# Kernel optimization log

Hardware: AMD Instinct MI355X
Metric: run time of the kernel (lower is better)

## Reference

```python
import jax, jax.numpy as jnp
import numpy as np

N_NODES = 400_000
N_EDGES = 1_600_000
N_GRAPHS = 16_384
MOL_DIM = 32
META_DIM = 16
HIDDEN = 64
NUM_SPECIES = 50
FUSION = 2 * HIDDEN + HIDDEN + 16  # mean+max pool (128) + meta (64) + species emb (16) = 208


def setup_inputs() -> dict:
    key = jax.random.key(0)
    ks = jax.random.split(key, 20)
    s = lambda *sh: sh
    inp = {
        "x": jax.random.normal(ks[0], (N_NODES, MOL_DIM), jnp.float32),
        "metadata": jax.random.normal(ks[1], (N_GRAPHS, META_DIM), jnp.float32),
        "edge_index": jax.random.randint(ks[2], (2, N_EDGES), 0, N_NODES),
        "batch": jnp.sort(jax.random.randint(ks[3], (N_NODES,), 0, N_GRAPHS)),
        "species_id": jax.random.randint(ks[4], (N_GRAPHS,), 0, NUM_SPECIES),
        # GCN layer params
        "W1": jax.random.normal(ks[5], (MOL_DIM, HIDDEN), jnp.float32) / np.sqrt(MOL_DIM),
        "b1": jnp.zeros((HIDDEN,), jnp.float32),
        "W2": jax.random.normal(ks[6], (HIDDEN, HIDDEN), jnp.float32) / np.sqrt(HIDDEN),
        "b2": jnp.zeros((HIDDEN,), jnp.float32),
        "W3": jax.random.normal(ks[7], (HIDDEN, HIDDEN), jnp.float32) / np.sqrt(HIDDEN),
        "b3": jnp.zeros((HIDDEN,), jnp.float32),
        # meta encoder
        "Wm": jax.random.normal(ks[8], (META_DIM, HIDDEN), jnp.float32) / np.sqrt(META_DIM),
        "bm": jnp.zeros((HIDDEN,), jnp.float32),
        "species_emb": jax.random.normal(ks[9], (NUM_SPECIES, 16), jnp.float32),
        # predictor
        "Wp1": jax.random.normal(ks[10], (FUSION, 64), jnp.float32) / np.sqrt(FUSION),
        "bp1": jnp.zeros((64,), jnp.float32),
        "Wp2": jax.random.normal(ks[11], (64, 1), jnp.float32) / 8.0,
        "bp2": jnp.zeros((1,), jnp.float32),
    }
    return inp


def _gcn_conv(x, W, b, row, col, dinv):
    # x' = D^{-1/2}(A+I)D^{-1/2} x W + b  (PyG GCNConv with self-loops)
    h = x @ W                                   # [N, out]
    norm = dinv[row] * dinv[col]                # [E]
    msg = norm[:, None] * h[col]                # [E, out]
    agg = jax.ops.segment_sum(msg, row, num_segments=x.shape[0])
    agg = agg + (dinv * dinv)[:, None] * h      # self-loop term
    return agg + b


def reference(x, metadata, edge_index, batch, species_id,
              W1, b1, W2, b2, W3, b3, Wm, bm, species_emb, Wp1, bp1, Wp2, bp2):
    row, col = edge_index[0], edge_index[1]
    deg = jax.ops.segment_sum(jnp.ones_like(row, jnp.float32), row,
                              num_segments=N_NODES) + 1.0  # +1 self loop
    dinv = jax.lax.rsqrt(deg)

    h = jax.nn.relu(_gcn_conv(x, W1, b1, row, col, dinv))
    h = jax.nn.relu(_gcn_conv(h, W2, b2, row, col, dinv))
    h = jax.nn.relu(_gcn_conv(h, W3, b3, row, col, dinv))

    counts = jax.ops.segment_sum(jnp.ones((N_NODES,), jnp.float32), batch,
                                 num_segments=N_GRAPHS)
    mean = jax.ops.segment_sum(h, batch, num_segments=N_GRAPHS) / \
           jnp.maximum(counts, 1.0)[:, None]
    mx = jax.ops.segment_max(h, batch, num_segments=N_GRAPHS)
    mx = jnp.where(counts[:, None] > 0, mx, 0.0)
    graph_embed = jnp.concatenate([mean, mx], axis=1)     # [G, 128]

    meta = jax.nn.relu(metadata @ Wm + bm)                 # [G, 64]
    meta_embed = jnp.concatenate([meta, species_emb[species_id]], axis=1)

    fused = jnp.concatenate([graph_embed, meta_embed], axis=1)  # [G, 208]
    out = jax.nn.relu(fused @ Wp1 + bp1) @ Wp2 + bp2       # dropout off (eval)
    return out
```

## Files before the change

kernel.cpp:

```cpp
#include <hip/hip_runtime.h>
#include <hip/hip_bf16.h>

#define N_NODES 400000
#define N_EDGES 1600000
#define N_GRAPHS 16384
#define CHUNK 32
#define NCHUNK (N_NODES / CHUNK)

#define BSHIFT 11
#define BKT_N (1 << BSHIFT)
#define NBKT ((N_NODES + BKT_N - 1) >> BSHIFT)
#define BIN_CHUNK 4096

typedef __attribute__((ext_vector_type(8))) short bf16x8;
typedef __attribute__((ext_vector_type(4))) float f32x4;
typedef unsigned short bfu;

__device__ __forceinline__ float rlane(float x, int k) {
    return __int_as_float(__builtin_amdgcn_readlane(__float_as_int(x), k));
}
__device__ __forceinline__ int rlanei(int x, int k) {
    return __builtin_amdgcn_readlane(x, k);
}

__device__ __forceinline__ short f2bf(float x) {
    unsigned u = __float_as_uint(x);
    unsigned r = (u + 0x7fffu + ((u >> 16) & 1u)) >> 16;
    return (short)r;
}
__device__ __forceinline__ float bf2f(short b) {
    return __uint_as_float(((unsigned)(unsigned short)b) << 16);
}
__device__ __forceinline__ float bfu2f(bfu b) {
    return __uint_as_float(((unsigned)b) << 16);
}

__global__ __launch_bounds__(256) void k_bcnt(const int* __restrict__ rows,
                                              int* __restrict__ bkt, int E) {
    __shared__ int l[NBKT];
    const int t = threadIdx.x;
    for (int i = t; i < NBKT; i += 256) l[i] = 0;
    __syncthreads();
    const int e0 = blockIdx.x * BIN_CHUNK;
#pragma unroll
    for (int k = 0; k < 16; ++k) {
        int e = e0 + k * 256 + t;
        if (e < E) atomicAdd(&l[rows[e] >> BSHIFT], 1);
    }
    __syncthreads();
    for (int i = t; i < NBKT; i += 256)
        if (l[i]) atomicAdd(&bkt[i], l[i]);
}

__global__ void k_bscan(const int* __restrict__ bkt, int* __restrict__ bbase,
                        int* __restrict__ bcur) {
    __shared__ int s[256];
    const int t = threadIdx.x;
    int v = (t < NBKT) ? bkt[t] : 0;
    s[t] = v; __syncthreads();
    for (int off = 1; off < 256; off <<= 1) {
        int x = (t >= off) ? s[t - off] : 0;
        __syncthreads();
        s[t] += x;
        __syncthreads();
    }
    int excl = s[t] - v;
    if (t < NBKT) { bbase[t] = excl; bcur[t] = excl; }
    if (t == NBKT) bbase[NBKT] = excl;
}

__global__ __launch_bounds__(256) void k_bin(const int* __restrict__ rows,
                                             const int* __restrict__ cols,
                                             int* __restrict__ bcur,
                                             int2* __restrict__ tmp, int E) {
    __shared__ int lcnt[NBKT];
    __shared__ int lbase[NBKT];
    const int t = threadIdx.x;
    const int e0 = blockIdx.x * BIN_CHUNK;
    for (int i = t; i < NBKT; i += 256) lcnt[i] = 0;
    __syncthreads();
    int r[16];
#pragma unroll
    for (int k = 0; k < 16; ++k) {
        int e = e0 + k * 256 + t;
        r[k] = (e < E) ? rows[e] : -1;
        if (r[k] >= 0) atomicAdd(&lcnt[r[k] >> BSHIFT], 1);
    }
    __syncthreads();
    for (int i = t; i < NBKT; i += 256) lbase[i] = atomicAdd(&bcur[i], lcnt[i]);
    __syncthreads();
    for (int i = t; i < NBKT; i += 256) lcnt[i] = 0;
    __syncthreads();
#pragma unroll
    for (int k = 0; k < 16; ++k) {
        int e = e0 + k * 256 + t;
        if (r[k] >= 0) {
            int b = r[k] >> BSHIFT;
            int p = lbase[b] + atomicAdd(&lcnt[b], 1);
            tmp[p] = make_int2(r[k], cols[e]);
        }
    }
}

__global__ __launch_bounds__(256) void k_csr(const int2* __restrict__ tmp,
                                             const int* __restrict__ bbase,
                                             int* __restrict__ row_ptr,
                                             float* __restrict__ dinv,
                                             int* __restrict__ colsOut,
                                             int N, int E) {
    __shared__ int lcnt[BKT_N];
    __shared__ int lofs[BKT_N];
    __shared__ int tsum[256];
    const int t = threadIdx.x;
    const int b = blockIdx.x;
    const int r0 = b << BSHIFT;
    const int S = bbase[b];
    const int T = bbase[b + 1];
    for (int i = t; i < BKT_N; i += 256) lcnt[i] = 0;
    __syncthreads();
    for (int e = S + t; e < T; e += 256) atomicAdd(&lcnt[tmp[e].x - r0], 1);
    __syncthreads();
    const int base8 = t * 8;
    int vals[8];
    int run = 0;
#pragma unroll
    for (int k = 0; k < 8; ++k) { vals[k] = run; run += lcnt[base8 + k]; }
    tsum[t] = run;
    __syncthreads();
    for (int off = 1; off < 256; off <<= 1) {
        int x = (t >= off) ? tsum[t - off] : 0;
        __syncthreads();
        tsum[t] += x;
        __syncthreads();
    }
    const int texcl = tsum[t] - run;
#pragma unroll
    for (int k = 0; k < 8; ++k) lofs[base8 + k] = texcl + vals[k];
    __syncthreads();
    for (int i = t; i < BKT_N; i += 256) {
        int node = r0 + i;
        if (node < N) {
            row_ptr[node] = S + lofs[i];
            dinv[node] = rsqrtf((float)lcnt[i] + 1.0f);
        }
    }
    if (b == 0 && t == 0) row_ptr[N] = E;
    __syncthreads();
    for (int e = S + t; e < T; e += 256) {
        int2 rc = tmp[e];
        int pos = S + atomicAdd(&lofs[rc.x - r0], 1);
        colsOut[pos] = rc.y;
    }
}

__global__ void k_gb(const int* __restrict__ batch, int* __restrict__ gstart,
                     int N, int G) {
    int i = blockIdx.x * blockDim.x + threadIdx.x;
    if (i <= N) {
        int b = (i < N) ? batch[i] : G;
        int prev = (i == 0) ? -1 : batch[i - 1];
        for (int g = prev + 1; g <= b; ++g) gstart[g] = i;
    }
}

template <int IN_D, bool PRESCALE, bool ABF16>
__global__ __launch_bounds__(256, 4) void k_gemm_mfma(
        const void* __restrict__ in_, const float* __restrict__ W,
        const float* __restrict__ dinv, bfu* __restrict__ out, int nTiles) {
    constexpr int KT = IN_D / 32;
    const int lane = threadIdx.x & 63;
    const int m = lane & 15;
    const int q = lane >> 4;

    bf16x8 Bhi[4][KT], Blo[4][KT];
#pragma unroll
    for (int nt = 0; nt < 4; ++nt) {
#pragma unroll
        for (int kt = 0; kt < KT; ++kt) {
#pragma unroll
            for (int j = 0; j < 8; ++j) {
                int k = kt * 32 + q * 8 + j;
                float w = W[k * 64 + nt * 16 + m];
                short hi = f2bf(w);
                Bhi[nt][kt][j] = hi;
                Blo[nt][kt][j] = f2bf(w - bf2f(hi));
            }
        }
    }

    const int wv = (blockIdx.x * 256 + threadIdx.x) >> 6;
    const int nwv = (gridDim.x * 256) >> 6;

    for (int tile = wv; tile < nTiles; tile += nwv) {
        const int node0 = tile * 16;
        f32x4 C[4];
#pragma unroll
        for (int nt = 0; nt < 4; ++nt) C[nt] = (f32x4){0.f, 0.f, 0.f, 0.f};

        if (ABF16) {
            const bfu* rowb = (const bfu*)in_ + (size_t)(node0 + m) * IN_D + q * 8;
            bf16x8 A[KT];
#pragma unroll
            for (int kt = 0; kt < KT; ++kt) A[kt] = *(const bf16x8*)(rowb + kt * 32);
#pragma unroll
            for (int nt = 0; nt < 4; ++nt) {
#pragma unroll
                for (int kt = 0; kt < KT; ++kt) {
                    C[nt] = __builtin_amdgcn_mfma_f32_16x16x32_bf16(A[kt], Bhi[nt][kt], C[nt], 0, 0, 0);
                    C[nt] = __builtin_amdgcn_mfma_f32_16x16x32_bf16(A[kt], Blo[nt][kt], C[nt], 0, 0, 0);
                }
            }
        } else {
            const float dv = PRESCALE ? dinv[node0 + m] : 1.0f;
            const float* rowp = (const float*)in_ + (size_t)(node0 + m) * IN_D + q * 8;
            bf16x8 Ahi[KT], Alo[KT];
#pragma unroll
            for (int kt = 0; kt < KT; ++kt) {
                f32x4 a0 = *(const f32x4*)(rowp + kt * 32);
                f32x4 a1 = *(const f32x4*)(rowp + kt * 32 + 4);
#pragma unroll
                for (int j = 0; j < 4; ++j) {
                    float xx = PRESCALE ? dv * a0[j] : a0[j];
                    short hi = f2bf(xx);
                    Ahi[kt][j] = hi;
                    Alo[kt][j] = f2bf(xx - bf2f(hi));
                }
#pragma unroll
                for (int j = 0; j < 4; ++j) {
                    float xx = PRESCALE ? dv * a1[j] : a1[j];
                    short hi = f2bf(xx);
                    Ahi[kt][4 + j] = hi;
                    Alo[kt][4 + j] = f2bf(xx - bf2f(hi));
                }
            }
#pragma unroll
            for (int nt = 0; nt < 4; ++nt) {
#pragma unroll
                for (int kt = 0; kt < KT; ++kt) {
                    C[nt] = __builtin_amdgcn_mfma_f32_16x16x32_bf16(Ahi[kt], Bhi[nt][kt], C[nt], 0, 0, 0);
                    C[nt] = __builtin_amdgcn_mfma_f32_16x16x32_bf16(Ahi[kt], Blo[nt][kt], C[nt], 0, 0, 0);
                    C[nt] = __builtin_amdgcn_mfma_f32_16x16x32_bf16(Alo[kt], Bhi[nt][kt], C[nt], 0, 0, 0);
                }
            }
        }

        bfu* op = out + (size_t)node0 * 64;
#pragma unroll
        for (int nt = 0; nt < 4; ++nt) {
#pragma unroll
            for (int r = 0; r < 4; ++r) {
                op[(size_t)(q * 4 + r) * 64 + nt * 16 + m] = (bfu)f2bf(C[nt][r]);
            }
        }
    }
}

template <int POOL>
__global__ __launch_bounds__(256, 8) void k_agg_seg(
        const bfu* __restrict__ M, const float* __restrict__ bias,
        const int* __restrict__ row_ptr, const int* __restrict__ cols,
        const float* __restrict__ dinv, const int* __restrict__ batch,
        bfu* __restrict__ out, float* __restrict__ psum,
        float* __restrict__ pmax) {
    const int lane = threadIdx.x & 63;
    int wid = (blockIdx.x * blockDim.x + threadIdx.x) >> 6;
    wid = __builtin_amdgcn_readfirstlane(wid);
    const int nw = (gridDim.x * blockDim.x) >> 6;
    const float b = bias[lane];
    const bfu* Ml = M + lane;

    for (int c = wid; c < NCHUNK; c += nw) {
        const int i0 = c * CHUNK;
        const int rpn = row_ptr[i0 + min(lane, CHUNK - 1) + 1];
        const int S = row_ptr[i0];
        const int ne = rlanei(rpn, CHUNK - 1) - S;
        const float dvv = dinv[i0 + min(lane, CHUNK - 1)];
        const int bvv = POOL ? batch[i0 + min(lane, CHUNK - 1)] : 0;

        int node = 0;
        int bnd = rlanei(rpn, 0) - S;
        float acc = 0.0f;
        float selfA = bfu2f(Ml[(size_t)i0 * 64]);
        float selfB = bfu2f(Ml[(size_t)(i0 + 1) * 64]);
        float selfC = bfu2f(Ml[(size_t)(i0 + 2) * 64]);
        int gcur = POOL ? rlanei(bvv, 0) : 0;
        float rsum = 0.0f, rmax = 0.0f;

        auto flush = [&]() {
            if (POOL) {
                atomicAdd(&psum[(size_t)gcur * 64 + lane], rsum);
                atomicMax((int*)&pmax[(size_t)gcur * 64 + lane], __float_as_int(rmax));
            }
        };
        auto finalize = [&]() {
            const float d = rlane(dvv, node);
            const float h = fmaxf(fmaf(d, selfA + acc, b), 0.0f);
            if (POOL) {
                const int g = rlanei(bvv, node);
                if (g != gcur) { flush(); gcur = g; rsum = 0.0f; rmax = 0.0f; }
                rsum += h;
                rmax = fmaxf(rmax, h);
            } else {
                out[(size_t)(i0 + node) * 64 + lane] = (bfu)f2bf(d * h);
            }
            acc = 0.0f;
            selfA = selfB;
            selfB = selfC;
            if (node + 3 < CHUNK) selfC = bfu2f(Ml[(size_t)(i0 + node + 3) * 64]);
            ++node;
            if (node < CHUNK) bnd = rlanei(rpn, node) - S;
        };

        if (ne > 0) {
            int bidx = 0;
            int a0 = S + lane, a1 = S + 64 + lane;
            int colv0 = (a0 < S + ne) ? cols[a0] : 0;
            int colv1 = (a1 < S + ne) ? cols[a1] : 0;
            unsigned ubuf[16];
#pragma unroll
            for (int k = 0; k < 16; ++k) {
                int e = min(k, ne - 1);
                int cc = rlanei(colv0, e);
                ubuf[k] = Ml[(size_t)cc * 64];
            }

            int j = 0;
            while (j + 16 <= ne) {
#pragma unroll
                for (int k = 0; k < 16; ++k) {
                    const int jj = j + k;
                    if ((jj & 63) == 0 && jj != 0) {
                        colv0 = colv1;
                        ++bidx;
                        int ad = S + (bidx + 1) * 64 + lane;
                        colv1 = (ad < S + ne) ? cols[ad] : 0;
                    }
                    while (jj == bnd) finalize();
                    acc += __uint_as_float(ubuf[k] << 16);
                    int ec = min(jj + 16, ne - 1);
                    int src = ((ec >> 6) == bidx) ? colv0 : colv1;
                    int cc = rlanei(src, ec & 63);
                    ubuf[k] = Ml[(size_t)cc * 64];
                }
                j += 16;
            }
            for (; j < ne; ++j) {
                while (j == bnd) finalize();
                acc += __uint_as_float(ubuf[j & 15] << 16);
            }
        }
        while (node < CHUNK) finalize();
        flush();
    }
}

__global__ __launch_bounds__(256) void k_asm(
        const float* __restrict__ psum, const float* __restrict__ pmax,
        const int* __restrict__ gstart, const float* __restrict__ metadata,
        const int* __restrict__ species, const float* __restrict__ emb,
        const float* __restrict__ Wm, const float* __restrict__ bm,
        float* __restrict__ fused, int G) {
    const int lane = threadIdx.x & 63;
    int wv = (blockIdx.x * blockDim.x + threadIdx.x) >> 6;
    const int nw = (gridDim.x * blockDim.x) >> 6;
    const float bmr = bm[lane];
    float wmr[16];
#pragma unroll
    for (int k = 0; k < 16; ++k) wmr[k] = Wm[k * 64 + lane];
    for (int g = wv; g < G; g += nw) {
        float gc = (float)(gstart[g + 1] - gstart[g]);
        float mean = psum[(size_t)g * 64 + lane] / fmaxf(gc, 1.0f);
        float mx = pmax[(size_t)g * 64 + lane];
        float md = lane < 16 ? metadata[(size_t)g * 16 + lane] : 0.0f;
        float mval = bmr;
#pragma unroll
        for (int k = 0; k < 16; ++k) mval = fmaf(rlane(md, k), wmr[k], mval);
        mval = fmaxf(mval, 0.0f);
        const int sid = species[g];
        float* fr = fused + (size_t)g * 224;
        fr[lane] = mean;
        fr[64 + lane] = mx;
        fr[128 + lane] = mval;
        if (lane < 16) fr[192 + lane] = emb[(size_t)sid * 16 + lane];
        else if (lane < 32) fr[192 + lane] = 0.0f;
    }
}

__global__ __launch_bounds__(256, 2) void k_pred_mfma(
        const float* __restrict__ fused, const float* __restrict__ Wp1,
        const float* __restrict__ bp1, const float* __restrict__ Wp2,
        const float* __restrict__ bp2, float* __restrict__ out, int G) {
    __shared__ __align__(16) short Whi[64 * 232];
    __shared__ __align__(16) short Wlo[64 * 232];
    const int t = threadIdx.x;
    for (int idx = t; idx < 64 * 232; idx += 256) {
        int n = idx / 232;
        int k = idx % 232;
        float w = (k < 208) ? Wp1[(size_t)k * 64 + n] : 0.0f;
        short hi = f2bf(w);
        Whi[n * 232 + k] = hi;
        Wlo[n * 232 + k] = f2bf(w - bf2f(hi));
    }
    __syncthreads();

    const int lane = t & 63;
    const int wave = t >> 6;
    const int m = lane & 15;
    const int q = lane >> 4;
    const int g0 = (blockIdx.x * 4 + wave) * 16;
    if (g0 >= G) return;

    const float* rowp = fused + (size_t)(g0 + m) * 224 + q * 8;

    f32x4 C[4];
#pragma unroll
    for (int nt = 0; nt < 4; ++nt) C[nt] = (f32x4){0.f, 0.f, 0.f, 0.f};

#pragma unroll
    for (int kt = 0; kt < 7; ++kt) {
        f32x4 a0 = *(const f32x4*)(rowp + kt * 32);
        f32x4 a1 = *(const f32x4*)(rowp + kt * 32 + 4);
        bf16x8 Ahi, Alo;
#pragma unroll
        for (int j = 0; j < 4; ++j) {
            short hi = f2bf(a0[j]);
            Ahi[j] = hi;
            Alo[j] = f2bf(a0[j] - bf2f(hi));
        }
#pragma unroll
        for (int j = 0; j < 4; ++j) {
            short hi = f2bf(a1[j]);
            Ahi[4 + j] = hi;
            Alo[4 + j] = f2bf(a1[j] - bf2f(hi));
        }
#pragma unroll
        for (int nt = 0; nt < 4; ++nt) {
            const int boff = (nt * 16 + m) * 232 + kt * 32 + q * 8;
            bf16x8 Bh = *(const bf16x8*)&Whi[boff];
            bf16x8 Bl = *(const bf16x8*)&Wlo[boff];
            C[nt] = __builtin_amdgcn_mfma_f32_16x16x32_bf16(Ahi, Bh, C[nt], 0, 0, 0);
            C[nt] = __builtin_amdgcn_mfma_f32_16x16x32_bf16(Ahi, Bl, C[nt], 0, 0, 0);
            C[nt] = __builtin_amdgcn_mfma_f32_16x16x32_bf16(Alo, Bh, C[nt], 0, 0, 0);
        }
    }

    float wp2r[4], bp1r[4];
#pragma unroll
    for (int nt = 0; nt < 4; ++nt) {
        wp2r[nt] = Wp2[nt * 16 + m];
        bp1r[nt] = bp1[nt * 16 + m];
    }
    const float bp2v = bp2[0];
    float s[4];
#pragma unroll
    for (int r = 0; r < 4; ++r) {
        float acc = 0.0f;
#pragma unroll
        for (int nt = 0; nt < 4; ++nt)
            acc += fmaxf(C[nt][r] + bp1r[nt], 0.0f) * wp2r[nt];
        s[r] = acc;
    }
#pragma unroll
    for (int off = 1; off < 16; off <<= 1) {
#pragma unroll
        for (int r = 0; r < 4; ++r) s[r] += __shfl_xor(s[r], off);
    }
    if (m == 0) {
#pragma unroll
        for (int r = 0; r < 4; ++r) out[g0 + q * 4 + r] = s[r] + bp2v;
    }
}

extern "C" void kernel_launch(void* const* d_in, const int* in_sizes, int n_in,
                              void* d_out, int out_size, void* d_ws, size_t ws_size,
                              hipStream_t stream) {
    const int N = N_NODES, E = N_EDGES, G = N_GRAPHS;

    const float* x        = (const float*)d_in[0];
    const float* metadata = (const float*)d_in[1];
    const int*   ei       = (const int*)d_in[2];
    const int*   batch    = (const int*)d_in[3];
    const int*   species  = (const int*)d_in[4];
    const float* W1 = (const float*)d_in[5];
    const float* b1 = (const float*)d_in[6];
    const float* W2 = (const float*)d_in[7];
    const float* b2 = (const float*)d_in[8];
    const float* W3 = (const float*)d_in[9];
    const float* b3 = (const float*)d_in[10];
    const float* Wm = (const float*)d_in[11];
    const float* bm = (const float*)d_in[12];
    const float* emb = (const float*)d_in[13];
    const float* Wp1 = (const float*)d_in[14];
    const float* bp1 = (const float*)d_in[15];
    const float* Wp2 = (const float*)d_in[16];
    const float* bp2 = (const float*)d_in[17];
    float* out = (float*)d_out;

    char* ws = (char*)d_ws;
    size_t off = 0;
    auto alloc = [&](size_t bytes) -> void* {
        void* p = ws + off;
        off = (off + bytes + 255) & ~(size_t)255;
        return p;
    };
    int*   row_ptr = (int*)alloc((size_t)(N + 1) * 4);
    float* dinv    = (float*)alloc((size_t)N * 4);
    int*   gstart  = (int*)alloc((size_t)(G + 1) * 4);
    int*   bkt     = (int*)alloc((size_t)NBKT * 4);
    int*   bbase   = (int*)alloc((size_t)(NBKT + 1) * 4);
    int*   bcur    = (int*)alloc((size_t)NBKT * 4);
    int*   colsS   = (int*)alloc((size_t)E * 4);
    float* psum    = (float*)alloc((size_t)G * 64 * 4);
    float* pmax    = (float*)alloc((size_t)G * 64 * 4);
    bfu*   Mb      = (bfu*)alloc((size_t)N * 64 * 2);
    bfu*   hb      = (bfu*)alloc((size_t)N * 64 * 2);
    float* fused   = (float*)alloc((size_t)G * 224 * 4);

    int2* tmp = (int2*)Mb;

    const int nbBin = (E + BIN_CHUNK - 1) / BIN_CHUNK;

    hipMemsetAsync(bkt, 0, (size_t)NBKT * 4, stream);
    hipMemsetAsync(psum, 0, (size_t)G * 64 * 4, stream);
    hipMemsetAsync(pmax, 0, (size_t)G * 64 * 4, stream);

    k_bcnt<<<nbBin, 256, 0, stream>>>(ei, bkt, E);
    k_bscan<<<1, 256, 0, stream>>>(bkt, bbase, bcur);
    k_bin<<<nbBin, 256, 0, stream>>>(ei, ei + E, bcur, tmp, E);
    k_csr<<<NBKT, 256, 0, stream>>>(tmp, bbase, row_ptr, dinv, colsS, N, E);
    k_gb<<<(N + 256) / 256 + 1, 256, 0, stream>>>(batch, gstart, N, G);

    const int nTiles = N / 16;
    k_gemm_mfma<32, true, false><<<1563, 256, 0, stream>>>(x, W1, dinv, Mb, nTiles);
    k_agg_seg<0><<<3125, 256, 0, stream>>>(Mb, b1, row_ptr, colsS, dinv, batch,
                                           hb, psum, pmax);
    k_gemm_mfma<64, false, true><<<1563, 256, 0, stream>>>(hb, W2, dinv, Mb, nTiles);
    k_agg_seg<0><<<3125, 256, 0, stream>>>(Mb, b2, row_ptr, colsS, dinv, batch,
                                           hb, psum, pmax);
    k_gemm_mfma<64, false, true><<<1563, 256, 0, stream>>>(hb, W3, dinv, Mb, nTiles);
    k_agg_seg<1><<<3125, 256, 0, stream>>>(Mb, b3, row_ptr, colsS, dinv, batch,
                                           hb, psum, pmax);

    k_asm<<<512, 256, 0, stream>>>(psum, pmax, gstart, metadata, species, emb, Wm, bm,
                                   fused, G);
    k_pred_mfma<<<(G / 16 + 3) / 4, 256, 0, stream>>>(fused, Wp1, bp1, Wp2, bp2, out, G);
}
```

Baseline: 488.3 us.

## Split wavefront into half-waves gathering two edges per step in aggregation

Rewrites the CSR aggregation kernel so each lane handles two bf16 features loaded as a packed 32-bit word, and the two half-waves gather different edges (even and odd) at the same time. Each gather instruction therefore covers two edge rows, halving the number of gather steps per edge list, and the half-wave partial sums are combined with a cross-half shuffle at each node finalize. This adds shuffles, more complex boundary handling when a node ends on an odd edge, and halves the lanes doing atomics and stores. Dynamic indexing of ubuf in the tail loop may spill to scratch.

Measured after the change: 541.0 us. +10.8%, slower.

```diff
diff --git a/kernel.cpp b/kernel.cpp
--- a/kernel.cpp
+++ b/kernel.cpp
@@ -263,11 +263,15 @@
         bfu* __restrict__ out, float* __restrict__ psum,
         float* __restrict__ pmax) {
     const int lane = threadIdx.x & 63;
+    const int c2 = lane & 31;
+    const bool hiHalf = lane >= 32;
     int wid = (blockIdx.x * blockDim.x + threadIdx.x) >> 6;
     wid = __builtin_amdgcn_readfirstlane(wid);
     const int nw = (gridDim.x * blockDim.x) >> 6;
-    const float b = bias[lane];
-    const bfu* Ml = M + lane;
+    const float bx = bias[2 * c2];
+    const float by = bias[2 * c2 + 1];
+    const unsigned* Mw = (const unsigned*)M;
+    unsigned* outU = (unsigned*)out;
 
     for (int c = wid; c < NCHUNK; c += nw) {
         const int i0 = c * CHUNK;
@@ -279,34 +283,45 @@
 
         int node = 0;
         int bnd = rlanei(rpn, 0) - S;
-        float acc = 0.0f;
-        float selfA = bfu2f(Ml[(size_t)i0 * 64]);
-        float selfB = bfu2f(Ml[(size_t)(i0 + 1) * 64]);
-        float selfC = bfu2f(Ml[(size_t)(i0 + 2) * 64]);
+        float accx = 0.f, accy = 0.f;
+        unsigned selfA = Mw[(size_t)i0 * 32 + c2];
+        unsigned selfB = Mw[(size_t)(i0 + 1) * 32 + c2];
+        unsigned selfC = Mw[(size_t)(i0 + 2) * 32 + c2];
         int gcur = POOL ? rlanei(bvv, 0) : 0;
-        float rsum = 0.0f, rmax = 0.0f;
+        float rsx = 0.f, rsy = 0.f, rmx = 0.f, rmy = 0.f;
 
         auto flush = [&]() {
-            if (POOL) {
-                atomicAdd(&psum[(size_t)gcur * 64 + lane], rsum);
-                atomicMax((int*)&pmax[(size_t)gcur * 64 + lane], __float_as_int(rmax));
+            if (POOL && lane < 32) {
+                float* pp = &psum[(size_t)gcur * 64 + 2 * c2];
+                atomicAdd(pp, rsx);
+                atomicAdd(pp + 1, rsy);
+                int* pm = (int*)&pmax[(size_t)gcur * 64 + 2 * c2];
+                atomicMax(pm, __float_as_int(rmx));
+                atomicMax(pm + 1, __float_as_int(rmy));
             }
         };
         auto finalize = [&]() {
             const float d = rlane(dvv, node);
-            const float h = fmaxf(fmaf(d, selfA + acc, b), 0.0f);
+            const float sx = accx + __shfl_xor(accx, 32);
+            const float sy = accy + __shfl_xor(accy, 32);
+            const float slo = __uint_as_float(selfA << 16);
+            const float shi = __uint_as_float(selfA & 0xFFFF0000u);
+            const float hx = fmaxf(fmaf(d, slo + sx, bx), 0.0f);
+            const float hy = fmaxf(fmaf(d, shi + sy, by), 0.0f);
             if (POOL) {
                 const int g = rlanei(bvv, node);
-                if (g != gcur) { flush(); gcur = g; rsum = 0.0f; rmax = 0.0f; }
-                rsum += h;
-                rmax = fmaxf(rmax, h);
+                if (g != gcur) { flush(); gcur = g; rsx = rsy = rmx = rmy = 0.f; }
+                rsx += hx; rsy += hy;
+                rmx = fmaxf(rmx, hx); rmy = fmaxf(rmy, hy);
             } else {
-                out[(size_t)(i0 + node) * 64 + lane] = (bfu)f2bf(d * h);
-            }
-            acc = 0.0f;
+                unsigned pk = (unsigned)(unsigned short)f2bf(d * hx)
+                            | ((unsigned)(unsigned short)f2bf(d * hy) << 16);
+                if (lane < 32) outU[(size_t)(i0 + node) * 32 + c2] = pk;
+            }
+            accx = 0.f; accy = 0.f;
             selfA = selfB;
             selfB = selfC;
-            if (node + 3 < CHUNK) selfC = bfu2f(Ml[(size_t)(i0 + node + 3) * 64]);
+            if (node + 3 < CHUNK) selfC = Mw[(size_t)(i0 + node + 3) * 32 + c2];
             ++node;
             if (node < CHUNK) bnd = rlanei(rpn, node) - S;
         };
@@ -319,34 +334,62 @@
             unsigned ubuf[16];
 #pragma unroll
             for (int k = 0; k < 16; ++k) {
-                int e = min(k, ne - 1);
-                int cc = rlanei(colv0, e);
-                ubuf[k] = Ml[(size_t)cc * 64];
+                int eE = min(2 * k, ne - 1);
+                int eO = min(2 * k + 1, ne - 1);
+                int ccE = rlanei(colv0, eE);
+                int ccO = rlanei(colv0, eO);
+                int cc = hiHalf ? ccO : ccE;
+                ubuf[k] = Mw[(size_t)cc * 32 + c2];
             }
 
             int j = 0;
-            while (j + 16 <= ne) {
+            while (j + 32 <= ne) {
+                if (j && !(j & 63)) {
+                    colv0 = colv1;
+                    ++bidx;
+                    int ad = S + (bidx + 1) * 64 + lane;
+                    colv1 = (ad < S + ne) ? cols[ad] : 0;
+                }
 #pragma unroll
                 for (int k = 0; k < 16; ++k) {
-                    const int jj = j + k;
-                    if ((jj & 63) == 0 && jj != 0) {
-                        colv0 = colv1;
-                        ++bidx;
-                        int ad = S + (bidx + 1) * 64 + lane;
-                        colv1 = (ad < S + ne) ? cols[ad] : 0;
+                    const int jj = j + 2 * k;
+                    const unsigned u = ubuf[k];
+                    int eE = min(jj + 32, ne - 1);
+                    int eO = min(jj + 33, ne - 1);
+                    int ccE = ((eE >> 6) == bidx) ? rlanei(colv0, eE & 63)
+                                                  : rlanei(colv1, eE & 63);
+                    int ccO = ((eO >> 6) == bidx) ? rlanei(colv0, eO & 63)
+                                                  : rlanei(colv1, eO & 63);
+                    int cc = hiHalf ? ccO : ccE;
+                    ubuf[k] = Mw[(size_t)cc * 32 + c2];
+                    const float vlo = __uint_as_float(u << 16);
+                    const float vhi = __uint_as_float(u & 0xFFFF0000u);
+                    while (jj == bnd) finalize();
+                    if (bnd == jj + 1) {
+                        if (!hiHalf) { accx += vlo; accy += vhi; }
+                        do { finalize(); } while (bnd == jj + 1);
+                        if (hiHalf) { accx += vlo; accy += vhi; }
+                    } else {
+                        accx += vlo; accy += vhi;
                     }
-                    while (jj == bnd) finalize();
-                    acc += __uint_as_float(ubuf[k] << 16);
-                    int ec = min(jj + 16, ne - 1);
-                    int src = ((ec >> 6) == bidx) ? colv0 : colv1;
-                    int cc = rlanei(src, ec & 63);
-                    ubuf[k] = Ml[(size_t)cc * 64];
-                }
-                j += 16;
-            }
-            for (; j < ne; ++j) {
-                while (j == bnd) finalize();
-                acc += __uint_as_float(ubuf[j & 15] << 16);
+                }
+                j += 32;
+            }
+            for (int e = j; e < ne; e += 2) {
+                const int k = (e - j) >> 1;
+                const unsigned u = ubuf[k];
+                const float vlo = __uint_as_float(u << 16);
+                const float vhi = __uint_as_float(u & 0xFFFF0000u);
+                while (e == bnd) finalize();
+                if (e + 1 >= ne) {
+                    if (!hiHalf) { accx += vlo; accy += vhi; }
+                } else if (bnd == e + 1) {
+                    if (!hiHalf) { accx += vlo; accy += vhi; }
+                    do { finalize(); } while (bnd == e + 1);
+                    if (hiHalf) { accx += vlo; accy += vhi; }
+                } else {
+                    accx += vlo; accy += vhi;
+                }
             }
         }
         while (node < CHUNK) finalize();
```

## Use atomic work-stealing for aggregation chunks and load column indices uniformly

Applied to the files above, without the earlier changes.

The aggregation kernel now has each wavefront fetch its next 32-node chunk from a global atomic counter (one counter per layer) instead of taking chunks in a fixed grid-stride order, and the grid shrinks to 2048 blocks. This is meant to balance load, since edge counts per chunk vary. Column indices are now read per edge with wave-uniform (scalar) loads instead of being staged in two 64-lane registers and broadcast with readlane, which drops the buffer-rotation logic. The column array is padded with 64 zeroed entries so prefetches past the end stay in bounds. The cost is one atomic per chunk plus more scalar memory traffic for the index reads.

Measured after the change: 1.091 ms. 124% more time.

```diff
diff --git a/kernel.cpp b/kernel.cpp
--- a/kernel.cpp
+++ b/kernel.cpp
@@ -261,18 +261,20 @@
         const int* __restrict__ row_ptr, const int* __restrict__ cols,
         const float* __restrict__ dinv, const int* __restrict__ batch,
         bfu* __restrict__ out, float* __restrict__ psum,
-        float* __restrict__ pmax) {
+        float* __restrict__ pmax, int* __restrict__ ctr) {
     const int lane = threadIdx.x & 63;
-    int wid = (blockIdx.x * blockDim.x + threadIdx.x) >> 6;
-    wid = __builtin_amdgcn_readfirstlane(wid);
-    const int nw = (gridDim.x * blockDim.x) >> 6;
     const float b = bias[lane];
     const bfu* Ml = M + lane;
 
-    for (int c = wid; c < NCHUNK; c += nw) {
+    for (;;) {
+        int cw = 0;
+        if (lane == 0) cw = atomicAdd(ctr, 1);
+        const int c = __builtin_amdgcn_readfirstlane(cw);
+        if (c >= NCHUNK) break;
+
         const int i0 = c * CHUNK;
         const int rpn = row_ptr[i0 + min(lane, CHUNK - 1) + 1];
-        const int S = row_ptr[i0];
+        const int S = __builtin_amdgcn_readfirstlane(row_ptr[i0]);
         const int ne = rlanei(rpn, CHUNK - 1) - S;
         const float dvv = dinv[i0 + min(lane, CHUNK - 1)];
         const int bvv = POOL ? batch[i0 + min(lane, CHUNK - 1)] : 0;
@@ -312,15 +314,10 @@
         };
 
         if (ne > 0) {
-            int bidx = 0;
-            int a0 = S + lane, a1 = S + 64 + lane;
-            int colv0 = (a0 < S + ne) ? cols[a0] : 0;
-            int colv1 = (a1 < S + ne) ? cols[a1] : 0;
             unsigned ubuf[16];
 #pragma unroll
             for (int k = 0; k < 16; ++k) {
-                int e = min(k, ne - 1);
-                int cc = rlanei(colv0, e);
+                const int cc = cols[S + k];
                 ubuf[k] = Ml[(size_t)cc * 64];
             }
 
@@ -329,17 +326,9 @@
 #pragma unroll
                 for (int k = 0; k < 16; ++k) {
                     const int jj = j + k;
-                    if ((jj & 63) == 0 && jj != 0) {
-                        colv0 = colv1;
-                        ++bidx;
-                        int ad = S + (bidx + 1) * 64 + lane;
-                        colv1 = (ad < S + ne) ? cols[ad] : 0;
-                    }
                     while (jj == bnd) finalize();
                     acc += __uint_as_float(ubuf[k] << 16);
-                    int ec = min(jj + 16, ne - 1);
-                    int src = ((ec >> 6) == bidx) ? colv0 : colv1;
-                    int cc = rlanei(src, ec & 63);
+                    const int cc = cols[S + jj + 16];
                     ubuf[k] = Ml[(size_t)cc * 64];
                 }
                 j += 16;
@@ -509,7 +498,8 @@
     int*   bkt     = (int*)alloc((size_t)NBKT * 4);
     int*   bbase   = (int*)alloc((size_t)(NBKT + 1) * 4);
     int*   bcur    = (int*)alloc((size_t)NBKT * 4);
-    int*   colsS   = (int*)alloc((size_t)E * 4);
+    int*   ctr     = (int*)alloc(3 * 4);
+    int*   colsS   = (int*)alloc((size_t)(E + 64) * 4);
     float* psum    = (float*)alloc((size_t)G * 64 * 4);
     float* pmax    = (float*)alloc((size_t)G * 64 * 4);
     bfu*   Mb      = (bfu*)alloc((size_t)N * 64 * 2);
@@ -521,6 +511,8 @@
     const int nbBin = (E + BIN_CHUNK - 1) / BIN_CHUNK;
 
     hipMemsetAsync(bkt, 0, (size_t)NBKT * 4, stream);
+    hipMemsetAsync(ctr, 0, 3 * 4, stream);
+    hipMemsetAsync(colsS + E, 0, 64 * 4, stream);
     hipMemsetAsync(psum, 0, (size_t)G * 64 * 4, stream);
     hipMemsetAsync(pmax, 0, (size_t)G * 64 * 4, stream);
 
@@ -532,14 +524,14 @@
 
     const int nTiles = N / 16;
     k_gemm_mfma<32, true, false><<<1563, 256, 0, stream>>>(x, W1, dinv, Mb, nTiles);
-    k_agg_seg<0><<<3125, 256, 0, stream>>>(Mb, b1, row_ptr, colsS, dinv, batch,
-                                           hb, psum, pmax);
+    k_agg_seg<0><<<2048, 256, 0, stream>>>(Mb, b1, row_ptr, colsS, dinv, batch,
+                                           hb, psum, pmax, ctr);
     k_gemm_mfma<64, false, true><<<1563, 256, 0, stream>>>(hb, W2, dinv, Mb, nTiles);
-    k_agg_seg<0><<<3125, 256, 0, stream>>>(Mb, b2, row_ptr, colsS, dinv, batch,
-                                           hb, psum, pmax);
+    k_agg_seg<0><<<2048, 256, 0, stream>>>(Mb, b2, row_ptr, colsS, dinv, batch,
+                                           hb, psum, pmax, ctr + 1);
     k_gemm_mfma<64, false, true><<<1563, 256, 0, stream>>>(hb, W3, dinv, Mb, nTiles);
-    k_agg_seg<1><<<3125, 256, 0, stream>>>(Mb, b3, row_ptr, colsS, dinv, batch,
-                                           hb, psum, pmax);
+    k_agg_seg<1><<<2048, 256, 0, stream>>>(Mb, b3, row_ptr, colsS, dinv, batch,
+                                           hb, psum, pmax, ctr + 2);
 
     k_asm<<<512, 256, 0, stream>>>(psum, pmax, gstart, metadata, species, emb, Wm, bm,
                                    fused, G);
```

## Interleave two node chunks per wave in GCN aggregation for more loads in flight

Applied to the files above, without the earlier changes.

The aggregation kernel now has each wave process two 32-node chunks at once. It alternates 16-edge gather blocks between two independent ring buffers, so twice as many gathers are outstanding per wave. Launch bounds drop from 8 to 4 waves per SIMD and the grid is halved to match. The grid-stride loop is removed and each wave handles exactly one chunk pair. The aim is more memory-level parallelism to hide gather latency, at the cost of more registers per wave, lower occupancy, and possible imbalance when the two chunks have different edge counts.

Result: slower. 631.8 us (+29.4%).

```diff
diff --git a/kernel.cpp b/kernel.cpp
--- a/kernel.cpp
+++ b/kernel.cpp
@@ -255,103 +255,123 @@
     }
 }
 
+
+#define AGG_FLUSH(sfx)                                                          \
+    if (POOL) {                                                                 \
+        atomicAdd(&psum[(size_t)gcur##sfx * 64 + lane], rsum##sfx);             \
+        atomicMax((int*)&pmax[(size_t)gcur##sfx * 64 + lane],                   \
+                  __float_as_int(rmax##sfx));                                   \
+    }
+
+#define AGG_FINALIZE(sfx) {                                                     \
+    const float d_ = rlane(dvv##sfx, node##sfx);                                \
+    const float h_ = fmaxf(fmaf(d_, selfA##sfx + acc##sfx, b), 0.0f);           \
+    if (POOL) {                                                                 \
+        const int g_ = rlanei(bvv##sfx, node##sfx);                             \
+        if (g_ != gcur##sfx) {                                                  \
+            AGG_FLUSH(sfx);                                                     \
+            gcur##sfx = g_; rsum##sfx = 0.0f; rmax##sfx = 0.0f;                 \
+        }                                                                       \
+        rsum##sfx += h_;                                                        \
+        rmax##sfx = fmaxf(rmax##sfx, h_);                                       \
+    } else {                                                                    \
+        out[(size_t)(i0##sfx + node##sfx) * 64 + lane] = (bfu)f2bf(d_ * h_);    \
+    }                                                                           \
+    acc##sfx = 0.0f;                                                            \
+    selfA##sfx = selfB##sfx;                                                    \
+    selfB##sfx = selfC##sfx;                                                    \
+    if (node##sfx + 3 < CHUNK)                                                  \
+        selfC##sfx = bfu2f(Ml[(size_t)(i0##sfx + node##sfx + 3) * 64]);         \
+    ++node##sfx;                                                                \
+    if (node##sfx < CHUNK) bnd##sfx = rlanei(rpn##sfx, node##sfx) - S##sfx; }
+
+#define AGG_INIT(sfx, cval)                                                     \
+    const int i0##sfx = (cval) * CHUNK;                                         \
+    const int rpn##sfx = row_ptr[i0##sfx + min(lane, CHUNK - 1) + 1];           \
+    const int S##sfx = row_ptr[i0##sfx];                                        \
+    const int ne##sfx = rlanei(rpn##sfx, CHUNK - 1) - S##sfx;                   \
+    const float dvv##sfx = dinv[i0##sfx + min(lane, CHUNK - 1)];                \
+    const int bvv##sfx = POOL ? batch[i0##sfx + min(lane, CHUNK - 1)] : 0;      \
+    int node##sfx = 0;                                                          \
+    int bnd##sfx = rlanei(rpn##sfx, 0) - S##sfx;                                \
+    float acc##sfx = 0.0f;                                                      \
+    float selfA##sfx = bfu2f(Ml[(size_t)i0##sfx * 64]);                         \
+    float selfB##sfx = bfu2f(Ml[(size_t)(i0##sfx + 1) * 64]);                   \
+    float selfC##sfx = bfu2f(Ml[(size_t)(i0##sfx + 2) * 64]);                   \
+    int gcur##sfx = POOL ? rlanei(bvv##sfx, 0) : 0;                             \
+    float rsum##sfx = 0.0f, rmax##sfx = 0.0f;                                   \
+    int bidx##sfx = 0;                                                          \
+    int colv0##sfx = 0, colv1##sfx = 0;                                         \
+    unsigned ubuf##sfx[16];                                                     \
+    int j##sfx = 0;
+
+#define AGG_RING_INIT(sfx)                                                      \
+    if (ne##sfx > 0) {                                                          \
+        int a0_ = S##sfx + lane, a1_ = S##sfx + 64 + lane;                      \
+        colv0##sfx = (a0_ < S##sfx + ne##sfx) ? cols[a0_] : 0;                  \
+        colv1##sfx = (a1_ < S##sfx + ne##sfx) ? cols[a1_] : 0;                  \
+        _Pragma("unroll")                                                       \
+        for (int k_ = 0; k_ < 16; ++k_) {                                       \
+            int e_ = min(k_, ne##sfx - 1);                                      \
+            int cc_ = rlanei(colv0##sfx, e_);                                   \
+            ubuf##sfx[k_] = Ml[(size_t)cc_ * 64];                               \
+        }                                                                       \
+    }
+
+#define AGG_BLOCK16(sfx) {                                                      \
+    _Pragma("unroll")                                                           \
+    for (int k_ = 0; k_ < 16; ++k_) {                                           \
+        const int jj_ = j##sfx + k_;                                            \
+        if ((jj_ & 63) == 0 && jj_ != 0) {                                      \
+            colv0##sfx = colv1##sfx;                                            \
+            ++bidx##sfx;                                                        \
+            int ad_ = S##sfx + (bidx##sfx + 1) * 64 + lane;                     \
+            colv1##sfx = (ad_ < S##sfx + ne##sfx) ? cols[ad_] : 0;              \
+        }                                                                       \
+        while (jj_ == bnd##sfx) AGG_FINALIZE(sfx);                              \
+        acc##sfx += __uint_as_float(ubuf##sfx[k_] << 16);                       \
+        int ec_ = min(jj_ + 16, ne##sfx - 1);                                   \
+        int src_ = ((ec_ >> 6) == bidx##sfx) ? colv0##sfx : colv1##sfx;         \
+        int cc_ = rlanei(src_, ec_ & 63);                                       \
+        ubuf##sfx[k_] = Ml[(size_t)cc_ * 64];                                   \
+    }                                                                           \
+    j##sfx += 16; }
+
+#define AGG_TAIL(sfx) {                                                         \
+    for (; j##sfx < ne##sfx; ++j##sfx) {                                        \
+        while (j##sfx == bnd##sfx) AGG_FINALIZE(sfx);                           \
+        acc##sfx += __uint_as_float(ubuf##sfx[j##sfx & 15] << 16);              \
+    }                                                                           \
+    while (node##sfx < CHUNK) AGG_FINALIZE(sfx);                                \
+    AGG_FLUSH(sfx); }
+
 template <int POOL>
-__global__ __launch_bounds__(256, 8) void k_agg_seg(
+__global__ __launch_bounds__(256, 4) void k_agg_seg(
         const bfu* __restrict__ M, const float* __restrict__ bias,
         const int* __restrict__ row_ptr, const int* __restrict__ cols,
         const float* __restrict__ dinv, const int* __restrict__ batch,
         bfu* __restrict__ out, float* __restrict__ psum,
         float* __restrict__ pmax) {
     const int lane = threadIdx.x & 63;
-    int wid = (blockIdx.x * blockDim.x + threadIdx.x) >> 6;
-    wid = __builtin_amdgcn_readfirstlane(wid);
-    const int nw = (gridDim.x * blockDim.x) >> 6;
     const float b = bias[lane];
     const bfu* Ml = M + lane;
 
-    for (int c = wid; c < NCHUNK; c += nw) {
-        const int i0 = c * CHUNK;
-        const int rpn = row_ptr[i0 + min(lane, CHUNK - 1) + 1];
-        const int S = row_ptr[i0];
-        const int ne = rlanei(rpn, CHUNK - 1) - S;
-        const float dvv = dinv[i0 + min(lane, CHUNK - 1)];
-        const int bvv = POOL ? batch[i0 + min(lane, CHUNK - 1)] : 0;
-
-        int node = 0;
-        int bnd = rlanei(rpn, 0) - S;
-        float acc = 0.0f;
-        float selfA = bfu2f(Ml[(size_t)i0 * 64]);
-        float selfB = bfu2f(Ml[(size_t)(i0 + 1) * 64]);
-        float selfC = bfu2f(Ml[(size_t)(i0 + 2) * 64]);
-        int gcur = POOL ? rlanei(bvv, 0) : 0;
-        float rsum = 0.0f, rmax = 0.0f;
-
-        auto flush = [&]() {
-            if (POOL) {
-                atomicAdd(&psum[(size_t)gcur * 64 + lane], rsum);
-                atomicMax((int*)&pmax[(size_t)gcur * 64 + lane], __float_as_int(rmax));
-            }
-        };
-        auto finalize = [&]() {
-            const float d = rlane(dvv, node);
-            const float h = fmaxf(fmaf(d, selfA + acc, b), 0.0f);
-            if (POOL) {
-                const int g = rlanei(bvv, node);
-                if (g != gcur) { flush(); gcur = g; rsum = 0.0f; rmax = 0.0f; }
-                rsum += h;
-                rmax = fmaxf(rmax, h);
-            } else {
-                out[(size_t)(i0 + node) * 64 + lane] = (bfu)f2bf(d * h);
-            }
-            acc = 0.0f;
-            selfA = selfB;
-            selfB = selfC;
-            if (node + 3 < CHUNK) selfC = bfu2f(Ml[(size_t)(i0 + node + 3) * 64]);
-            ++node;
-            if (node < CHUNK) bnd = rlanei(rpn, node) - S;
-        };
-
-        if (ne > 0) {
-            int bidx = 0;
-            int a0 = S + lane, a1 = S + 64 + lane;
-            int colv0 = (a0 < S + ne) ? cols[a0] : 0;
-            int colv1 = (a1 < S + ne) ? cols[a1] : 0;
-            unsigned ubuf[16];
-#pragma unroll
-            for (int k = 0; k < 16; ++k) {
-                int e = min(k, ne - 1);
-                int cc = rlanei(colv0, e);
-                ubuf[k] = Ml[(size_t)cc * 64];
-            }
-
-            int j = 0;
-            while (j + 16 <= ne) {
-#pragma unroll
-                for (int k = 0; k < 16; ++k) {
-                    const int jj = j + k;
-                    if ((jj & 63) == 0 && jj != 0) {
-                        colv0 = colv1;
-                        ++bidx;
-                        int ad = S + (bidx + 1) * 64 + lane;
-                        colv1 = (ad < S + ne) ? cols[ad] : 0;
-                    }
-                    while (jj == bnd) finalize();
-                    acc += __uint_as_float(ubuf[k] << 16);
-                    int ec = min(jj + 16, ne - 1);
-                    int src = ((ec >> 6) == bidx) ? colv0 : colv1;
-                    int cc = rlanei(src, ec & 63);
-                    ubuf[k] = Ml[(size_t)cc * 64];
-                }
-                j += 16;
-            }
-            for (; j < ne; ++j) {
-                while (j == bnd) finalize();
-                acc += __uint_as_float(ubuf[j & 15] << 16);
-            }
-        }
-        while (node < CHUNK) finalize();
-        flush();
-    }
+    const int w = (blockIdx.x * 256 + threadIdx.x) >> 6;
+    if (2 * w >= NCHUNK) return;
+
+    AGG_INIT(A, 2 * w);
+    AGG_RING_INIT(A);
+    AGG_INIT(B, 2 * w + 1);
+    AGG_RING_INIT(B);
+
+    while (jA + 16 <= neA && jB + 16 <= neB) {
+        AGG_BLOCK16(A);
+        AGG_BLOCK16(B);
+    }
+    while (jA + 16 <= neA) AGG_BLOCK16(A);
+    while (jB + 16 <= neB) AGG_BLOCK16(B);
+    AGG_TAIL(A);
+    AGG_TAIL(B);
 }
 
 __global__ __launch_bounds__(256) void k_asm(
@@ -531,15 +551,16 @@
     k_gb<<<(N + 256) / 256 + 1, 256, 0, stream>>>(batch, gstart, N, G);
 
     const int nTiles = N / 16;
+    const int nbAgg = 1563;
     k_gemm_mfma<32, true, false><<<1563, 256, 0, stream>>>(x, W1, dinv, Mb, nTiles);
-    k_agg_seg<0><<<3125, 256, 0, stream>>>(Mb, b1, row_ptr, colsS, dinv, batch,
-                                           hb, psum, pmax);
+    k_agg_seg<0><<<nbAgg, 256, 0, stream>>>(Mb, b1, row_ptr, colsS, dinv, batch,
+                                            hb, psum, pmax);
     k_gemm_mfma<64, false, true><<<1563, 256, 0, stream>>>(hb, W2, dinv, Mb, nTiles);
-    k_agg_seg<0><<<3125, 256, 0, stream>>>(Mb, b2, row_ptr, colsS, dinv, batch,
-                                           hb, psum, pmax);
+    k_agg_seg<0><<<nbAgg, 256, 0, stream>>>(Mb, b2, row_ptr, colsS, dinv, batch,
+                                            hb, psum, pmax);
     k_gemm_mfma<64, false, true><<<1563, 256, 0, stream>>>(hb, W3, dinv, Mb, nTiles);
-    k_agg_seg<1><<<3125, 256, 0, stream>>>(Mb, b3, row_ptr, colsS, dinv, batch,
-                                           hb, psum, pmax);
+    k_agg_seg<1><<<nbAgg, 256, 0, stream>>>(Mb, b3, row_ptr, colsS, dinv, batch,
+                                            hb, psum, pmax);
 
     k_asm<<<512, 256, 0, stream>>>(psum, pmax, gstart, metadata, species, emb, Wm, bm,
                                    fused, G);
```
